# Performance work log

Measured on AMD Instinct MI355X. Metric: run time of the kernel, lower is better.

Reference implementation:

```python
import jax, jax.numpy as jnp
import numpy as np
from jax import lax

# Faithful JAX port of the approxmatch CUDA kernel (Fan et al. EMD):
#   iterates annealing levels j = 7 .. -2 with level = -4^j (0 at j=-2),
#   alternately normalizing transport weights by remaining source capacity
#   (remainL) and capping by remaining target capacity (remainR).
# Cost = sum over matched pairs of Euclidean (sqrt) distance * match weight.

def _approx_match(xyz1, xyz2):
    # xyz1: (b,n,3), xyz2: (b,m,3)
    b, n, _ = xyz1.shape
    m = xyz2.shape[1]
    # squared pairwise distances (b,n,m) -- computed once, reused every level
    d2 = jnp.sum((xyz1[:, :, None, :] - xyz2[:, None, :, :]) ** 2, axis=-1)
    # CUDA kernel capacities: multiL = max(1, m/n), multiR = max(1, n/m) (int ratios)
    multiL = float(max(1, m // n))
    multiR = float(max(1, n // m))
    remainL = jnp.full((b, n), multiL, dtype=xyz1.dtype)
    remainR = jnp.full((b, m), multiR, dtype=xyz1.dtype)
    match = jnp.zeros((b, n, m), dtype=xyz1.dtype)

    # levels for j = 7..-1 are -4^j; j = -2 uses level = 0
    levels = jnp.concatenate([
        -(4.0 ** jnp.arange(7, -2, -1, dtype=jnp.float32)),
        jnp.zeros((1,), jnp.float32),
    ])

    def body(carry, level):
        match, remainL, remainR = carry
        w = jnp.exp(level * d2) * remainR[:, None, :]                 # (b,n,m)
        w = w * (remainL / (1e-9 + w.sum(axis=2)))[:, :, None]        # normalize rows, scale by L capacity
        r = jnp.minimum(remainR / (1e-9 + w.sum(axis=1)), 1.0)        # cap columns by R capacity
        w = w * r[:, None, :]
        match = match + w
        remainL = jnp.maximum(remainL - w.sum(axis=2), 0.0)
        remainR = jnp.maximum(remainR - w.sum(axis=1), 0.0)
        return (match, remainL, remainR), None

    (match, _, _), _ = lax.scan(body, (match, remainL, remainR), levels)
    return match, d2


def _match_cost(match, d2):
    # matchcost kernel: sum_{k,l} match[k,l] * sqrt(||xyz1_k - xyz2_l||^2)
    dist = jnp.sqrt(jnp.maximum(d2, 1e-30))
    return jnp.sum(match * dist, axis=(1, 2))  # (b,)


def setup_inputs() -> dict:
    key = jax.random.key(0)
    k1, k2 = jax.random.split(key)
    b, n, m = 8, 2048, 2048
    input1 = jax.random.uniform(k1, (b, n, 3), dtype=jnp.float32)
    input2 = jax.random.uniform(k2, (b, m, 3), dtype=jnp.float32)
    return {"input1": input1, "input2": input2}


def reference(input1, input2):
    match, d2 = _approx_match(input1, input2)
    return _match_cost(match, d2)  # (b,) per-batch EMD cost
```

## Files before the change

kernel.cpp:

```cpp
#include <hip/hip_runtime.h>
#include <math.h>


#define NPTS 2048
#define BLOCK 256
#define RPW 4
#define RPB ((BLOCK / 64) * RPW)
#define L2E 1.4426950408889634f

__device__ __forceinline__ float xreduce(float v) {
#pragma unroll
    for (int off = 1; off < 64; off <<= 1) v += __shfl_xor(v, off, 64);
    return v;
}
__device__ __forceinline__ float fexp2(float x) { return __builtin_amdgcn_exp2f(x); }
__device__ __forceinline__ float fsqrt(float x) { return __builtin_amdgcn_sqrtf(x); }

__global__ __launch_bounds__(BLOCK, 4) void k_A(
    const float* __restrict__ xyz1, const float* __restrict__ xyz2,
    float4* __restrict__ p1w, float4* __restrict__ p2w,
    float* __restrict__ f_g, float kk, float multiL, float multiR)
{
    __shared__ float sx[NPTS], sy[NPTS], sz[NPTS], sb[NPTS];
    const int row0 = blockIdx.x * RPB;
    const int batch = row0 >> 11;
    const int rloc = row0 & 2047;
    const float* g1 = xyz1 + (size_t)batch * NPTS * 3;
    const float* g2 = xyz2 + (size_t)batch * NPTS * 3;
    if (threadIdx.x < RPB) {
        int i = rloc + threadIdx.x;
        p1w[((size_t)batch << 11) + i] = make_float4(g1[3*i], g1[3*i+1], g1[3*i+2], 0.f);
    } else if (threadIdx.x < 2 * RPB) {
        int i = rloc + threadIdx.x - RPB;
        p2w[((size_t)batch << 11) + i] = make_float4(g2[3*i], g2[3*i+1], g2[3*i+2], 0.f);
    }
    for (int j = threadIdx.x; j < NPTS; j += BLOCK) {
        float qx = g2[3*j], qy = g2[3*j+1], qz = g2[3*j+2];
        sx[j] = qx; sy[j] = qy; sz[j] = qz;
        sb[j] = kk * (qx*qx + qy*qy + qz*qz);
    }
    __syncthreads();
    const int lane = threadIdx.x & 63;
    const int r0 = row0 + (threadIdx.x >> 6) * RPW;
    float pxp[RPW], pyp[RPW], pzp[RPW], pa[RPW], acc[RPW];
#pragma unroll
    for (int r = 0; r < RPW; ++r) {
        const float* p = g1 + 3 * ((r0 & 2047) + r);
        float x = p[0], y = p[1], z = p[2];
        pa[r] = kk * (x*x + y*y + z*z);
        pxp[r] = -2.f*kk*x; pyp[r] = -2.f*kk*y; pzp[r] = -2.f*kk*z;
        acc[r] = 0.f;
    }
    for (int j = lane; j < NPTS; j += 64) {
        float qx = sx[j], qy = sy[j], qz = sz[j], qb = sb[j];
#pragma unroll
        for (int r = 0; r < RPW; ++r) {
            float t = pa[r] + qb;
            t = fmaf(pxp[r], qx, fmaf(pyp[r], qy, fmaf(pzp[r], qz, t)));
            acc[r] += fexp2(t);
        }
    }
#pragma unroll
    for (int r = 0; r < RPW; ++r) {
        float s = multiR * xreduce(acc[r]);
        if (lane == 0) f_g[r0 + r] = multiL / (1e-9f + s);
    }
}

template <bool FIRST>
__global__ __launch_bounds__(BLOCK, 4) void k_B(
    const float4* __restrict__ p1w, const float4* __restrict__ p2w,
    const float* __restrict__ f_g, float* __restrict__ remR,
    float* __restrict__ c_g, float kk, float multiR)
{
    __shared__ float sx[NPTS], sy[NPTS], sz[NPTS], sb[NPTS], sf[NPTS];
    const int col0 = blockIdx.x * RPB;
    const int batch = col0 >> 11;
    const float4* P1 = p1w + ((size_t)batch << 11);
    const float* F = f_g + ((size_t)batch << 11);
    for (int i = threadIdx.x; i < NPTS; i += BLOCK) {
        float4 q = P1[i];
        sx[i] = q.x; sy[i] = q.y; sz[i] = q.z;
        sb[i] = kk * (q.x*q.x + q.y*q.y + q.z*q.z);
        sf[i] = F[i];
    }
    __syncthreads();
    const int lane = threadIdx.x & 63;
    const int c0 = col0 + (threadIdx.x >> 6) * RPW;
    float cxp[RPW], cyp[RPW], czp[RPW], ca[RPW], acc[RPW];
#pragma unroll
    for (int r = 0; r < RPW; ++r) {
        float4 q = p2w[c0 + r];
        ca[r] = kk * (q.x*q.x + q.y*q.y + q.z*q.z);
        cxp[r] = -2.f*kk*q.x; cyp[r] = -2.f*kk*q.y; czp[r] = -2.f*kk*q.z;
        acc[r] = 0.f;
    }
    for (int i = lane; i < NPTS; i += 64) {
        float qx = sx[i], qy = sy[i], qz = sz[i], qb = sb[i], w = sf[i];
#pragma unroll
        for (int r = 0; r < RPW; ++r) {
            float t = ca[r] + qb;
            t = fmaf(cxp[r], qx, fmaf(cyp[r], qy, fmaf(czp[r], qz, t)));
            acc[r] = fmaf(w, fexp2(t), acc[r]);
        }
    }
#pragma unroll
    for (int r = 0; r < RPW; ++r) {
        float s = xreduce(acc[r]);
        if (lane == 0) {
            int gj = c0 + r;
            float R = FIRST ? multiR : remR[gj];
            float colsum = R * s;
            float rr = fminf(R / (1e-9f + colsum), 1.0f);
            c_g[gj] = R * rr;
            remR[gj] = fmaxf(R - colsum * rr, 0.f);
        }
    }
}

template <int MODE, bool FIRSTC>
__global__ __launch_bounds__(BLOCK, 4) void k_CA(
    const float4* __restrict__ p1w, const float4* __restrict__ p2w,
    float* __restrict__ f_g, const float* __restrict__ c_g,
    const float* __restrict__ remR, float* __restrict__ remL,
    float* __restrict__ costrow, float kp, float invkp, float multiL)
{
    __shared__ float sx[NPTS], sy[NPTS], sz[NPTS], sc[NPTS], sr[NPTS];
    const int row0 = blockIdx.x * RPB;
    const int batch = row0 >> 11;
    const float4* P2 = p2w + ((size_t)batch << 11);
    const float* C = c_g + ((size_t)batch << 11);
    const float* R = remR + ((size_t)batch << 11);
    for (int j = threadIdx.x; j < NPTS; j += BLOCK) {
        float4 q = P2[j];
        sx[j] = q.x; sy[j] = q.y; sz[j] = q.z; sc[j] = C[j];
        if (MODE) sr[j] = R[j];
    }
    __syncthreads();
    const int lane = threadIdx.x & 63;
    const int r0 = row0 + (threadIdx.x >> 6) * RPW;
    float pxp[RPW], pyp[RPW], pzp[RPW], pa[RPW];
    float aT[RPW], aU[RPW], aA[RPW];
    float aAs = 0.f;
#pragma unroll
    for (int r = 0; r < RPW; ++r) {
        float4 q = p1w[r0 + r];
        if (MODE == 0) { pxp[r] = q.x; pyp[r] = q.y; pzp[r] = q.z; pa[r] = 0.f; }
        else {
            pa[r] = kp * (q.x*q.x + q.y*q.y + q.z*q.z);
            pxp[r] = -2.f*kp*q.x; pyp[r] = -2.f*kp*q.y; pzp[r] = -2.f*kp*q.z;
        }
        aT[r] = 0.f; aU[r] = 0.f; aA[r] = 0.f;
    }
    for (int j = lane; j < NPTS; j += 64) {
        float qx = sx[j], qy = sy[j], qz = sz[j], cw = sc[j];
        if (MODE == 0) {
#pragma unroll
            for (int r = 0; r < RPW; ++r) {
                float dx = pxp[r] - qx, dy = pyp[r] - qy, dz = pzp[r] - qz;
                float d2 = fmaf(dx, dx, fmaf(dy, dy, dz * dz));
                aT[r] += cw;
                aU[r] = fmaf(cw, fsqrt(d2), aU[r]);
            }
        } else {
            float qb = kp * fmaf(qx, qx, fmaf(qy, qy, qz * qz));
            float rw = sr[j];
            if (MODE == 2) aAs += rw;
#pragma unroll
            for (int r = 0; r < RPW; ++r) {
                float t = pa[r] + qb;
                t = fmaf(pxp[r], qx, fmaf(pyp[r], qy, fmaf(pzp[r], qz, t)));
                float e1 = fexp2(t);
                float e4;
                if (MODE == 1) { float e2 = e1 * e1; e4 = e2 * e2; } else e4 = e1;
                float d2 = fmaxf(t * invkp, 0.f);
                float eC = cw * e4;
                aT[r] += eC;
                aU[r] = fmaf(eC, fsqrt(d2), aU[r]);
                if (MODE == 1) aA[r] = fmaf(rw, e1, aA[r]);
            }
        }
    }
    float aas = (MODE == 2) ? xreduce(aAs) : 0.f;
#pragma unroll
    for (int r = 0; r < RPW; ++r) {
        float tt = xreduce(aT[r]);
        float uu = xreduce(aU[r]);
        float aa = (MODE == 1) ? xreduce(aA[r]) : aas;
        if (lane == 0) {
            int gi = r0 + r;
            float fi = f_g[gi];
            float rl0 = FIRSTC ? multiL : remL[gi];
            float rl = fmaxf(rl0 - fi * tt, 0.f);
            float cst = FIRSTC ? 0.f : costrow[gi];
            costrow[gi] = cst + fi * uu;
            remL[gi] = rl;
            if (MODE) f_g[gi] = rl / (1e-9f + aa);
        }
    }
}

__global__ void k_cost(const float* __restrict__ costrow,
                       float* __restrict__ out, int n) {
    __shared__ float wsum[BLOCK / 64];
    const float* cr = costrow + (size_t)blockIdx.x * n;
    float s = 0.f;
    for (int i = threadIdx.x; i < n; i += BLOCK) s += cr[i];
    s = xreduce(s);
    int wave = threadIdx.x >> 6, lane = threadIdx.x & 63;
    if (lane == 0) wsum[wave] = s;
    __syncthreads();
    if (threadIdx.x == 0) {
        float t = 0.f;
#pragma unroll
        for (int w = 0; w < BLOCK / 64; ++w) t += wsum[w];
        out[blockIdx.x] = t;
    }
}

extern "C" void kernel_launch(void* const* d_in, const int* in_sizes, int n_in,
                              void* d_out, int out_size, void* d_ws, size_t ws_size,
                              hipStream_t stream) {
    const float* xyz1 = (const float*)d_in[0];
    const float* xyz2 = (const float*)d_in[1];
    float* out = (float*)d_out;
    const int b = out_size;
    const int n = in_sizes[0] / (3 * b);
    const int m = in_sizes[1] / (3 * b);
    const int bn = b * n, bm = b * m;

    float4* p1w = (float4*)d_ws;
    float4* p2w = p1w + bn;
    float* remL    = (float*)(p2w + bm);
    float* remR    = remL + bn;
    float* f       = remR + bm;
    float* c       = f + bn;
    float* costrow = c + bm;

    const float multiL = (float)((m / n > 1) ? (m / n) : 1);
    const float multiR = (float)((n / m > 1) ? (n / m) : 1);

    dim3 g(bn / RPB), blk(BLOCK);
    const float kk0 = -16384.f * L2E;
    k_A<<<g, blk, 0, stream>>>(xyz1, xyz2, p1w, p2w, f, kk0, multiL, multiR);

    for (int t = 0; t < 10; ++t) {
        const float lvl = (t < 9) ? -exp2f(2.f * (float)(7 - t)) : 0.f;
        const float kk = lvl * L2E;
        if (t == 0)
            k_B<true><<<g, blk, 0, stream>>>(p1w, p2w, f, remR, c, kk, multiR);
        else
            k_B<false><<<g, blk, 0, stream>>>(p1w, p2w, f, remR, c, kk, multiR);

        if (t == 0) {
            float kp = kk * 0.25f;
            k_CA<1, true><<<g, blk, 0, stream>>>(p1w, p2w, f, c, remR, remL,
                                                 costrow, kp, 1.f / kp, multiL);
        } else if (t < 8) {
            float kp = kk * 0.25f;
            k_CA<1, false><<<g, blk, 0, stream>>>(p1w, p2w, f, c, remR, remL,
                                                  costrow, kp, 1.f / kp, multiL);
        } else if (t == 8) {
            k_CA<2, false><<<g, blk, 0, stream>>>(p1w, p2w, f, c, remR, remL,
                                                  costrow, kk, 1.f / kk, multiL);
        } else {
            k_CA<0, false><<<g, blk, 0, stream>>>(p1w, p2w, f, c, remR, remL,
                                                  costrow, 0.f, 0.f, multiL);
        }
    }
    k_cost<<<dim3(b), blk, 0, stream>>>(costrow, out, n);
}
```

Before: 327.8 us.

## Fuse column-sum pass into row kernel via shared and global atomics

Drops the separate column-pass kernel (k_B) per annealing level. The row kernel now does a second pass that recomputes the exponentials weighted by the new row factors. It reduces these per column in LDS with atomics and accumulates into a double-buffered global sigma array. A thin elementwise kernel then applies the column capping. The level-zero step replaces the per-column work with a broadcast sum, and the final cost reduction is folded into the last row kernel with atomics to the output. In exchange, each row kernel does extra exp work and issues many global atomics, and the summation order is no longer deterministic.

```diff
diff --git a/kernel.cpp b/kernel.cpp
--- a/kernel.cpp
+++ b/kernel.cpp
@@ -5,7 +5,7 @@
 #define NPTS 2048
 #define BLOCK 256
 #define RPW 4
-#define RPB ((BLOCK / 64) * RPW)
+#define RPB 16
 #define L2E 1.4426950408889634f
 
 __device__ __forceinline__ float xreduce(float v) {
@@ -16,12 +16,20 @@
 __device__ __forceinline__ float fexp2(float x) { return __builtin_amdgcn_exp2f(x); }
 __device__ __forceinline__ float fsqrt(float x) { return __builtin_amdgcn_sqrtf(x); }
 
-__global__ __launch_bounds__(BLOCK, 4) void k_A(
+__global__ void k_zero(float* __restrict__ sig2, float* __restrict__ out,
+                       int nsig, int nout) {
+    int i = blockIdx.x * BLOCK + threadIdx.x;
+    if (i < nsig) sig2[i] = 0.f;
+    if (i < nout) out[i] = 0.f;
+}
+
+__global__ __launch_bounds__(BLOCK, 4) void k_A0(
     const float* __restrict__ xyz1, const float* __restrict__ xyz2,
     float4* __restrict__ p1w, float4* __restrict__ p2w,
-    float* __restrict__ f_g, float kk, float multiL, float multiR)
+    float* __restrict__ f_g, float* __restrict__ sig,
+    float kk, float multiL, float multiR)
 {
-    __shared__ float sx[NPTS], sy[NPTS], sz[NPTS], sb[NPTS];
+    __shared__ float sx[NPTS], sy[NPTS], sz[NPTS], sm[NPTS];
     const int row0 = blockIdx.x * RPB;
     const int batch = row0 >> 11;
     const int rloc = row0 & 2047;
@@ -35,87 +43,68 @@
         p2w[((size_t)batch << 11) + i] = make_float4(g2[3*i], g2[3*i+1], g2[3*i+2], 0.f);
     }
     for (int j = threadIdx.x; j < NPTS; j += BLOCK) {
-        float qx = g2[3*j], qy = g2[3*j+1], qz = g2[3*j+2];
-        sx[j] = qx; sy[j] = qy; sz[j] = qz;
-        sb[j] = kk * (qx*qx + qy*qy + qz*qz);
+        sx[j] = g2[3*j]; sy[j] = g2[3*j+1]; sz[j] = g2[3*j+2];
+        sm[j] = 0.f;
     }
     __syncthreads();
     const int lane = threadIdx.x & 63;
-    const int r0 = row0 + (threadIdx.x >> 6) * RPW;
-    float pxp[RPW], pyp[RPW], pzp[RPW], pa[RPW], acc[RPW];
-#pragma unroll
-    for (int r = 0; r < RPW; ++r) {
-        const float* p = g1 + 3 * ((r0 & 2047) + r);
+    const int wave = threadIdx.x >> 6;
+    const int r0 = row0 + wave * RPW;
+    float pa[RPW], pxp[RPW], pyp[RPW], pzp[RPW], acc[RPW];
+#pragma unroll
+    for (int r = 0; r < RPW; ++r) {
+        const float* p = g1 + 3 * (rloc + wave * RPW + r);
         float x = p[0], y = p[1], z = p[2];
         pa[r] = kk * (x*x + y*y + z*z);
         pxp[r] = -2.f*kk*x; pyp[r] = -2.f*kk*y; pzp[r] = -2.f*kk*z;
         acc[r] = 0.f;
     }
     for (int j = lane; j < NPTS; j += 64) {
-        float qx = sx[j], qy = sy[j], qz = sz[j], qb = sb[j];
+        float qx = sx[j], qy = sy[j], qz = sz[j];
+        float qb = kk * fmaf(qx, qx, fmaf(qy, qy, qz * qz));
 #pragma unroll
         for (int r = 0; r < RPW; ++r) {
-            float t = pa[r] + qb;
-            t = fmaf(pxp[r], qx, fmaf(pyp[r], qy, fmaf(pzp[r], qz, t)));
+            float t = fmaf(pxp[r], qx, fmaf(pyp[r], qy, fmaf(pzp[r], qz, pa[r] + qb)));
             acc[r] += fexp2(t);
         }
     }
+    float fp[RPW];
 #pragma unroll
     for (int r = 0; r < RPW; ++r) {
         float s = multiR * xreduce(acc[r]);
-        if (lane == 0) f_g[r0 + r] = multiL / (1e-9f + s);
-    }
+        fp[r] = multiL / (1e-9f + s);
+        if (lane == 0) f_g[r0 + r] = fp[r];
+    }
+    for (int it = 0; it < NPTS / 64; ++it) {
+        int j = (wave * 512 + it * 64 + lane) & 2047;
+        float qx = sx[j], qy = sy[j], qz = sz[j];
+        float qb = kk * fmaf(qx, qx, fmaf(qy, qy, qz * qz));
+        float part = 0.f;
+#pragma unroll
+        for (int r = 0; r < RPW; ++r) {
+            float t = fmaf(pxp[r], qx, fmaf(pyp[r], qy, fmaf(pzp[r], qz, pa[r] + qb)));
+            part = fmaf(fp[r], fexp2(t), part);
+        }
+        atomicAdd(&sm[j], part);
+    }
+    __syncthreads();
+    float* sg = sig + ((size_t)batch << 11);
+    for (int j = threadIdx.x; j < NPTS; j += BLOCK)
+        atomicAdd(&sg[j], sm[j]);
 }
 
 template <bool FIRST>
-__global__ __launch_bounds__(BLOCK, 4) void k_B(
-    const float4* __restrict__ p1w, const float4* __restrict__ p2w,
-    const float* __restrict__ f_g, float* __restrict__ remR,
-    float* __restrict__ c_g, float kk, float multiR)
+__global__ void k_thin(float* __restrict__ sig, float* __restrict__ remR,
+                       float* __restrict__ c_g, float multiR)
 {
-    __shared__ float sx[NPTS], sy[NPTS], sz[NPTS], sb[NPTS], sf[NPTS];
-    const int col0 = blockIdx.x * RPB;
-    const int batch = col0 >> 11;
-    const float4* P1 = p1w + ((size_t)batch << 11);
-    const float* F = f_g + ((size_t)batch << 11);
-    for (int i = threadIdx.x; i < NPTS; i += BLOCK) {
-        float4 q = P1[i];
-        sx[i] = q.x; sy[i] = q.y; sz[i] = q.z;
-        sb[i] = kk * (q.x*q.x + q.y*q.y + q.z*q.z);
-        sf[i] = F[i];
-    }
-    __syncthreads();
-    const int lane = threadIdx.x & 63;
-    const int c0 = col0 + (threadIdx.x >> 6) * RPW;
-    float cxp[RPW], cyp[RPW], czp[RPW], ca[RPW], acc[RPW];
-#pragma unroll
-    for (int r = 0; r < RPW; ++r) {
-        float4 q = p2w[c0 + r];
-        ca[r] = kk * (q.x*q.x + q.y*q.y + q.z*q.z);
-        cxp[r] = -2.f*kk*q.x; cyp[r] = -2.f*kk*q.y; czp[r] = -2.f*kk*q.z;
-        acc[r] = 0.f;
-    }
-    for (int i = lane; i < NPTS; i += 64) {
-        float qx = sx[i], qy = sy[i], qz = sz[i], qb = sb[i], w = sf[i];
-#pragma unroll
-        for (int r = 0; r < RPW; ++r) {
-            float t = ca[r] + qb;
-            t = fmaf(cxp[r], qx, fmaf(cyp[r], qy, fmaf(czp[r], qz, t)));
-            acc[r] = fmaf(w, fexp2(t), acc[r]);
-        }
-    }
-#pragma unroll
-    for (int r = 0; r < RPW; ++r) {
-        float s = xreduce(acc[r]);
-        if (lane == 0) {
-            int gj = c0 + r;
-            float R = FIRST ? multiR : remR[gj];
-            float colsum = R * s;
-            float rr = fminf(R / (1e-9f + colsum), 1.0f);
-            c_g[gj] = R * rr;
-            remR[gj] = fmaxf(R - colsum * rr, 0.f);
-        }
-    }
+    int idx = blockIdx.x * BLOCK + threadIdx.x;
+    float s = sig[idx];
+    sig[idx] = 0.f;
+    float R = FIRST ? multiR : remR[idx];
+    float colsum = R * s;
+    float rr = fminf(R / (1e-9f + colsum), 1.0f);
+    c_g[idx] = R * rr;
+    remR[idx] = fmaxf(R - colsum * rr, 0.f);
 }
 
 template <int MODE, bool FIRSTC>
@@ -123,7 +112,8 @@
     const float4* __restrict__ p1w, const float4* __restrict__ p2w,
     float* __restrict__ f_g, const float* __restrict__ c_g,
     const float* __restrict__ remR, float* __restrict__ remL,
-    float* __restrict__ costrow, float kp, float invkp, float multiL)
+    float* __restrict__ costrow, float* __restrict__ sig,
+    float kp, float rsqkp, float multiL)
 {
     __shared__ float sx[NPTS], sy[NPTS], sz[NPTS], sc[NPTS], sr[NPTS];
     const int row0 = blockIdx.x * RPB;
@@ -133,89 +123,130 @@
     const float* R = remR + ((size_t)batch << 11);
     for (int j = threadIdx.x; j < NPTS; j += BLOCK) {
         float4 q = P2[j];
+        sx[j] = q.x; sy[j] = q.y; sz[j] = q.z; sc[j] = C[j]; sr[j] = R[j];
+    }
+    __syncthreads();
+    const int lane = threadIdx.x & 63;
+    const int wave = threadIdx.x >> 6;
+    const int r0 = row0 + wave * RPW;
+    float pa[RPW], pxp[RPW], pyp[RPW], pzp[RPW], fi[RPW];
+    float aT[RPW], aU[RPW], aA[RPW], aAs = 0.f;
+#pragma unroll
+    for (int r = 0; r < RPW; ++r) {
+        float4 q = p1w[r0 + r];
+        pa[r] = kp * (q.x*q.x + q.y*q.y + q.z*q.z);
+        pxp[r] = -2.f*kp*q.x; pyp[r] = -2.f*kp*q.y; pzp[r] = -2.f*kp*q.z;
+        fi[r] = f_g[r0 + r];
+        aT[r] = 0.f; aU[r] = 0.f; aA[r] = 0.f;
+    }
+    for (int j = lane; j < NPTS; j += 64) {
+        float qx = sx[j], qy = sy[j], qz = sz[j], cw = sc[j], rw = sr[j];
+        float qb = kp * fmaf(qx, qx, fmaf(qy, qy, qz * qz));
+        if (MODE == 2) aAs += rw;
+#pragma unroll
+        for (int r = 0; r < RPW; ++r) {
+            float t = fmaf(pxp[r], qx, fmaf(pyp[r], qy, fmaf(pzp[r], qz, pa[r] + qb)));
+            float e1 = fexp2(t);
+            float eC;
+            if (MODE == 1) { float e2 = e1 * e1; eC = cw * (e2 * e2); }
+            else           { eC = cw * e1; }
+            aT[r] += eC;
+            aU[r] = fmaf(eC, fsqrt(fabsf(t)), aU[r]);
+            if (MODE == 1) aA[r] = fmaf(rw, e1, aA[r]);
+        }
+    }
+    float aas = (MODE == 2) ? xreduce(aAs) : 0.f;
+    float fp[RPW];
+#pragma unroll
+    for (int r = 0; r < RPW; ++r) {
+        float tt = xreduce(aT[r]);
+        float uu = xreduce(aU[r]) * rsqkp;
+        float aa = (MODE == 1) ? xreduce(aA[r]) : aas;
+        int gi = r0 + r;
+        float rl0 = FIRSTC ? multiL : remL[gi];
+        float rl = fmaxf(rl0 - fi[r] * tt, 0.f);
+        fp[r] = rl / (1e-9f + aa);
+        if (lane == 0) {
+            costrow[gi] = (FIRSTC ? 0.f : costrow[gi]) + fi[r] * uu;
+            remL[gi] = rl;
+            f_g[gi] = fp[r];
+        }
+    }
+    __syncthreads();
+    for (int j = threadIdx.x; j < NPTS; j += BLOCK) sc[j] = 0.f;
+    __syncthreads();
+    if (MODE == 1) {
+        for (int it = 0; it < NPTS / 64; ++it) {
+            int j = (wave * 512 + it * 64 + lane) & 2047;
+            float qx = sx[j], qy = sy[j], qz = sz[j];
+            float qb = kp * fmaf(qx, qx, fmaf(qy, qy, qz * qz));
+            float part = 0.f;
+#pragma unroll
+            for (int r = 0; r < RPW; ++r) {
+                float t = fmaf(pxp[r], qx, fmaf(pyp[r], qy, fmaf(pzp[r], qz, pa[r] + qb)));
+                part = fmaf(fp[r], fexp2(t), part);
+            }
+            atomicAdd(&sc[j], part);
+        }
+    } else {
+        if (lane == 0) atomicAdd(&sc[0], fp[0] + fp[1] + fp[2] + fp[3]);
+    }
+    __syncthreads();
+    float* sg = sig + ((size_t)batch << 11);
+    if (MODE == 1) {
+        for (int j = threadIdx.x; j < NPTS; j += BLOCK)
+            atomicAdd(&sg[j], sc[j]);
+    } else {
+        float bc = sc[0];
+        for (int j = threadIdx.x; j < NPTS; j += BLOCK)
+            atomicAdd(&sg[j], bc);
+    }
+}
+
+__global__ __launch_bounds__(BLOCK, 4) void k_C9(
+    const float4* __restrict__ p1w, const float4* __restrict__ p2w,
+    const float* __restrict__ f_g, const float* __restrict__ c_g,
+    const float* __restrict__ costrow, float* __restrict__ out)
+{
+    __shared__ float sx[NPTS], sy[NPTS], sz[NPTS], sc[NPTS];
+    __shared__ float wsum[BLOCK / 64];
+    const int row0 = blockIdx.x * RPB;
+    const int batch = row0 >> 11;
+    const float4* P2 = p2w + ((size_t)batch << 11);
+    const float* C = c_g + ((size_t)batch << 11);
+    for (int j = threadIdx.x; j < NPTS; j += BLOCK) {
+        float4 q = P2[j];
         sx[j] = q.x; sy[j] = q.y; sz[j] = q.z; sc[j] = C[j];
-        if (MODE) sr[j] = R[j];
     }
     __syncthreads();
     const int lane = threadIdx.x & 63;
-    const int r0 = row0 + (threadIdx.x >> 6) * RPW;
-    float pxp[RPW], pyp[RPW], pzp[RPW], pa[RPW];
-    float aT[RPW], aU[RPW], aA[RPW];
-    float aAs = 0.f;
+    const int wave = threadIdx.x >> 6;
+    const int r0 = row0 + wave * RPW;
+    float px[RPW], py[RPW], pz[RPW], aU[RPW];
 #pragma unroll
     for (int r = 0; r < RPW; ++r) {
         float4 q = p1w[r0 + r];
-        if (MODE == 0) { pxp[r] = q.x; pyp[r] = q.y; pzp[r] = q.z; pa[r] = 0.f; }
-        else {
-            pa[r] = kp * (q.x*q.x + q.y*q.y + q.z*q.z);
-            pxp[r] = -2.f*kp*q.x; pyp[r] = -2.f*kp*q.y; pzp[r] = -2.f*kp*q.z;
-        }
-        aT[r] = 0.f; aU[r] = 0.f; aA[r] = 0.f;
+        px[r] = q.x; py[r] = q.y; pz[r] = q.z; aU[r] = 0.f;
     }
     for (int j = lane; j < NPTS; j += 64) {
         float qx = sx[j], qy = sy[j], qz = sz[j], cw = sc[j];
-        if (MODE == 0) {
-#pragma unroll
-            for (int r = 0; r < RPW; ++r) {
-                float dx = pxp[r] - qx, dy = pyp[r] - qy, dz = pzp[r] - qz;
-                float d2 = fmaf(dx, dx, fmaf(dy, dy, dz * dz));
-                aT[r] += cw;
-                aU[r] = fmaf(cw, fsqrt(d2), aU[r]);
-            }
-        } else {
-            float qb = kp * fmaf(qx, qx, fmaf(qy, qy, qz * qz));
-            float rw = sr[j];
-            if (MODE == 2) aAs += rw;
-#pragma unroll
-            for (int r = 0; r < RPW; ++r) {
-                float t = pa[r] + qb;
-                t = fmaf(pxp[r], qx, fmaf(pyp[r], qy, fmaf(pzp[r], qz, t)));
-                float e1 = fexp2(t);
-                float e4;
-                if (MODE == 1) { float e2 = e1 * e1; e4 = e2 * e2; } else e4 = e1;
-                float d2 = fmaxf(t * invkp, 0.f);
-                float eC = cw * e4;
-                aT[r] += eC;
-                aU[r] = fmaf(eC, fsqrt(d2), aU[r]);
-                if (MODE == 1) aA[r] = fmaf(rw, e1, aA[r]);
-            }
-        }
-    }
-    float aas = (MODE == 2) ? xreduce(aAs) : 0.f;
-#pragma unroll
-    for (int r = 0; r < RPW; ++r) {
-        float tt = xreduce(aT[r]);
+#pragma unroll
+        for (int r = 0; r < RPW; ++r) {
+            float dx = px[r] - qx, dy = py[r] - qy, dz = pz[r] - qz;
+            float d2 = fmaf(dx, dx, fmaf(dy, dy, dz * dz));
+            aU[r] = fmaf(cw, fsqrt(d2), aU[r]);
+        }
+    }
+    float psum = 0.f;
+#pragma unroll
+    for (int r = 0; r < RPW; ++r) {
         float uu = xreduce(aU[r]);
-        float aa = (MODE == 1) ? xreduce(aA[r]) : aas;
-        if (lane == 0) {
-            int gi = r0 + r;
-            float fi = f_g[gi];
-            float rl0 = FIRSTC ? multiL : remL[gi];
-            float rl = fmaxf(rl0 - fi * tt, 0.f);
-            float cst = FIRSTC ? 0.f : costrow[gi];
-            costrow[gi] = cst + fi * uu;
-            remL[gi] = rl;
-            if (MODE) f_g[gi] = rl / (1e-9f + aa);
-        }
-    }
-}
-
-__global__ void k_cost(const float* __restrict__ costrow,
-                       float* __restrict__ out, int n) {
-    __shared__ float wsum[BLOCK / 64];
-    const float* cr = costrow + (size_t)blockIdx.x * n;
-    float s = 0.f;
-    for (int i = threadIdx.x; i < n; i += BLOCK) s += cr[i];
-    s = xreduce(s);
-    int wave = threadIdx.x >> 6, lane = threadIdx.x & 63;
-    if (lane == 0) wsum[wave] = s;
-    __syncthreads();
-    if (threadIdx.x == 0) {
-        float t = 0.f;
-#pragma unroll
-        for (int w = 0; w < BLOCK / 64; ++w) t += wsum[w];
-        out[blockIdx.x] = t;
-    }
+        if (lane == 0) psum += costrow[r0 + r] + f_g[r0 + r] * uu;
+    }
+    if (lane == 0) wsum[wave] = psum;
+    __syncthreads();
+    if (threadIdx.x == 0)
+        atomicAdd(&out[batch], wsum[0] + wsum[1] + wsum[2] + wsum[3]);
 }
 
 extern "C" void kernel_launch(void* const* d_in, const int* in_sizes, int n_in,
@@ -231,42 +262,47 @@
 
     float4* p1w = (float4*)d_ws;
     float4* p2w = p1w + bn;
-    float* remL    = (float*)(p2w + bm);
-    float* remR    = remL + bn;
+    float* remR    = (float*)(p2w + bm);
     float* f       = remR + bm;
     float* c       = f + bn;
-    float* costrow = c + bm;
+    float* remL    = c + bm;
+    float* costrow = remL + bn;
+    float* sig     = costrow + bn;
 
     const float multiL = (float)((m / n > 1) ? (m / n) : 1);
     const float multiR = (float)((n / m > 1) ? (n / m) : 1);
 
-    dim3 g(bn / RPB), blk(BLOCK);
+    dim3 blk(BLOCK);
+    dim3 gFat(bn / RPB), gThin(bm / BLOCK);
+
+    k_zero<<<dim3((2 * bm + BLOCK - 1) / BLOCK), blk, 0, stream>>>(sig, out, 2 * bm, b);
+
     const float kk0 = -16384.f * L2E;
-    k_A<<<g, blk, 0, stream>>>(xyz1, xyz2, p1w, p2w, f, kk0, multiL, multiR);
+    k_A0<<<gFat, blk, 0, stream>>>(xyz1, xyz2, p1w, p2w, f, sig, kk0, multiL, multiR);
 
     for (int t = 0; t < 10; ++t) {
-        const float lvl = (t < 9) ? -exp2f(2.f * (float)(7 - t)) : 0.f;
-        const float kk = lvl * L2E;
-        if (t == 0)
-            k_B<true><<<g, blk, 0, stream>>>(p1w, p2w, f, remR, c, kk, multiR);
-        else
-            k_B<false><<<g, blk, 0, stream>>>(p1w, p2w, f, remR, c, kk, multiR);
-
-        if (t == 0) {
-            float kp = kk * 0.25f;
-            k_CA<1, true><<<g, blk, 0, stream>>>(p1w, p2w, f, c, remR, remL,
-                                                 costrow, kp, 1.f / kp, multiL);
-        } else if (t < 8) {
-            float kp = kk * 0.25f;
-            k_CA<1, false><<<g, blk, 0, stream>>>(p1w, p2w, f, c, remR, remL,
-                                                  costrow, kp, 1.f / kp, multiL);
+        float* sigR = sig + (size_t)(t & 1) * bm;
+        float* sigW = sig + (size_t)((t + 1) & 1) * bm;
+        if (t == 0) k_thin<true><<<gThin, blk, 0, stream>>>(sigR, remR, c, multiR);
+        else        k_thin<false><<<gThin, blk, 0, stream>>>(sigR, remR, c, multiR);
+
+        if (t < 8) {
+            const float kk = -exp2f(2.f * (float)(7 - t)) * L2E;
+            const float kp = kk * 0.25f;
+            const float rsq = 1.f / sqrtf(-kp);
+            if (t == 0)
+                k_CA<1, true><<<gFat, blk, 0, stream>>>(p1w, p2w, f, c, remR, remL,
+                                                        costrow, sigW, kp, rsq, multiL);
+            else
+                k_CA<1, false><<<gFat, blk, 0, stream>>>(p1w, p2w, f, c, remR, remL,
+                                                         costrow, sigW, kp, rsq, multiL);
         } else if (t == 8) {
-            k_CA<2, false><<<g, blk, 0, stream>>>(p1w, p2w, f, c, remR, remL,
-                                                  costrow, kk, 1.f / kk, multiL);
+            const float kp = -0.25f * L2E;
+            const float rsq = 1.f / sqrtf(0.25f * L2E);
+            k_CA<2, false><<<gFat, blk, 0, stream>>>(p1w, p2w, f, c, remR, remL,
+                                                     costrow, sigW, kp, rsq, multiL);
         } else {
-            k_CA<0, false><<<g, blk, 0, stream>>>(p1w, p2w, f, c, remR, remL,
-                                                  costrow, 0.f, 0.f, multiL);
-        }
-    }
-    k_cost<<<dim3(b), blk, 0, stream>>>(costrow, out, n);
-}
+            k_C9<<<gFat, blk, 0, stream>>>(p1w, p2w, f, c, costrow, out);
+        }
+    }
+}
```

Measured after the change: 590.3 us. +80.1%, slower.

## Use packed float2 FMAs for exponent terms and fold sqrt scaling out of loop

Applied to the files above, without the earlier changes.

Rewrites the inner loops of the row, column and update kernels to process pairs of rows with two-wide vector FMAs, so the compiler can emit packed FP32 instructions. In the update kernel, the distance is taken as sqrt(|t|) and the 1/sqrt(-kp) factor is applied once after the reduction instead of multiplying by 1/kp per element. It also drops the launch-bounds occupancy hint, adds unroll pragmas, and special-cases the final level kernel. For the t==8 level, the diff recomputes kp on the host as -0.25*L2E and uses the non-squared exponent, so it must still match the original level-1 weights. The absolute-value trick can change rounding near zero distance.

```diff
diff --git a/kernel.cpp b/kernel.cpp
--- a/kernel.cpp
+++ b/kernel.cpp
@@ -4,19 +4,37 @@
 
 #define NPTS 2048
 #define BLOCK 256
-#define RPW 4
-#define RPB ((BLOCK / 64) * RPW)
+#define RPB 16
 #define L2E 1.4426950408889634f
 
+typedef float v2 __attribute__((ext_vector_type(2)));
+
+__device__ __forceinline__ float fexp2(float x) { return __builtin_amdgcn_exp2f(x); }
+__device__ __forceinline__ float fsqrt(float x) { return __builtin_amdgcn_sqrtf(x); }
+__device__ __forceinline__ v2 fma2(v2 a, v2 b, v2 c) { return __builtin_elementwise_fma(a, b, c); }
+__device__ __forceinline__ v2 sp(float a) { v2 r; r.x = a; r.y = a; return r; }
 __device__ __forceinline__ float xreduce(float v) {
 #pragma unroll
     for (int off = 1; off < 64; off <<= 1) v += __shfl_xor(v, off, 64);
     return v;
 }
-__device__ __forceinline__ float fexp2(float x) { return __builtin_amdgcn_exp2f(x); }
-__device__ __forceinline__ float fsqrt(float x) { return __builtin_amdgcn_sqrtf(x); }
-
-__global__ __launch_bounds__(BLOCK, 4) void k_A(
+
+struct RowPair {
+    v2 pa, px, py, pz;
+};
+__device__ __forceinline__ RowPair mk_pair(float4 a, float4 b, float kp) {
+    RowPair r;
+    r.pa = v2{kp * a.w, kp * b.w};
+    r.px = v2{-2.f*kp*a.x, -2.f*kp*b.x};
+    r.py = v2{-2.f*kp*a.y, -2.f*kp*b.y};
+    r.pz = v2{-2.f*kp*a.z, -2.f*kp*b.z};
+    return r;
+}
+__device__ __forceinline__ v2 term(const RowPair& r, float qx, float qy, float qz, v2 qb2) {
+    return fma2(r.px, sp(qx), fma2(r.py, sp(qy), fma2(r.pz, sp(qz), r.pa + qb2)));
+}
+
+__global__ __launch_bounds__(BLOCK) void k_A(
     const float* __restrict__ xyz1, const float* __restrict__ xyz2,
     float4* __restrict__ p1w, float4* __restrict__ p2w,
     float* __restrict__ f_g, float kk, float multiL, float multiR)
@@ -41,34 +59,37 @@
     }
     __syncthreads();
     const int lane = threadIdx.x & 63;
-    const int r0 = row0 + (threadIdx.x >> 6) * RPW;
-    float pxp[RPW], pyp[RPW], pzp[RPW], pa[RPW], acc[RPW];
-#pragma unroll
-    for (int r = 0; r < RPW; ++r) {
-        const float* p = g1 + 3 * ((r0 & 2047) + r);
-        float x = p[0], y = p[1], z = p[2];
-        pa[r] = kk * (x*x + y*y + z*z);
-        pxp[r] = -2.f*kk*x; pyp[r] = -2.f*kk*y; pzp[r] = -2.f*kk*z;
-        acc[r] = 0.f;
-    }
+    const int wave = threadIdx.x >> 6;
+    const int r0 = row0 + wave * 4;
+    RowPair rA, rB;
+    {
+        const float* p = g1 + 3 * ((r0 & 2047));
+        float4 p0 = make_float4(p[0], p[1], p[2], p[0]*p[0]+p[1]*p[1]+p[2]*p[2]);
+        float4 p1 = make_float4(p[3], p[4], p[5], p[3]*p[3]+p[4]*p[4]+p[5]*p[5]);
+        float4 p2 = make_float4(p[6], p[7], p[8], p[6]*p[6]+p[7]*p[7]+p[8]*p[8]);
+        float4 p3 = make_float4(p[9], p[10], p[11], p[9]*p[9]+p[10]*p[10]+p[11]*p[11]);
+        rA = mk_pair(p0, p1, kk); rB = mk_pair(p2, p3, kk);
+    }
+    v2 aSA = sp(0.f), aSB = sp(0.f);
+#pragma unroll 8
     for (int j = lane; j < NPTS; j += 64) {
-        float qx = sx[j], qy = sy[j], qz = sz[j], qb = sb[j];
-#pragma unroll
-        for (int r = 0; r < RPW; ++r) {
-            float t = pa[r] + qb;
-            t = fmaf(pxp[r], qx, fmaf(pyp[r], qy, fmaf(pzp[r], qz, t)));
-            acc[r] += fexp2(t);
-        }
-    }
-#pragma unroll
-    for (int r = 0; r < RPW; ++r) {
-        float s = multiR * xreduce(acc[r]);
-        if (lane == 0) f_g[r0 + r] = multiL / (1e-9f + s);
+        float qx = sx[j], qy = sy[j], qz = sz[j];
+        v2 qb2 = sp(sb[j]);
+        v2 tA = term(rA, qx, qy, qz, qb2);
+        v2 tB = term(rB, qx, qy, qz, qb2);
+        aSA += v2{fexp2(tA.x), fexp2(tA.y)};
+        aSB += v2{fexp2(tB.x), fexp2(tB.y)};
+    }
+    float sv[4] = {xreduce(aSA.x), xreduce(aSA.y), xreduce(aSB.x), xreduce(aSB.y)};
+    if (lane == 0) {
+#pragma unroll
+        for (int r = 0; r < 4; ++r)
+            f_g[r0 + r] = multiL / (1e-9f + multiR * sv[r]);
     }
 }
 
 template <bool FIRST>
-__global__ __launch_bounds__(BLOCK, 4) void k_B(
+__global__ __launch_bounds__(BLOCK) void k_B(
     const float4* __restrict__ p1w, const float4* __restrict__ p2w,
     const float* __restrict__ f_g, float* __restrict__ remR,
     float* __restrict__ c_g, float kk, float multiR)
@@ -86,31 +107,35 @@
     }
     __syncthreads();
     const int lane = threadIdx.x & 63;
-    const int c0 = col0 + (threadIdx.x >> 6) * RPW;
-    float cxp[RPW], cyp[RPW], czp[RPW], ca[RPW], acc[RPW];
-#pragma unroll
-    for (int r = 0; r < RPW; ++r) {
-        float4 q = p2w[c0 + r];
-        ca[r] = kk * (q.x*q.x + q.y*q.y + q.z*q.z);
-        cxp[r] = -2.f*kk*q.x; cyp[r] = -2.f*kk*q.y; czp[r] = -2.f*kk*q.z;
-        acc[r] = 0.f;
-    }
+    const int wave = threadIdx.x >> 6;
+    const int c0 = col0 + wave * 4;
+    RowPair rA, rB;
+    {
+        float4 q0 = p2w[c0], q1 = p2w[c0+1], q2 = p2w[c0+2], q3 = p2w[c0+3];
+        q0.w = q0.x*q0.x + q0.y*q0.y + q0.z*q0.z;
+        q1.w = q1.x*q1.x + q1.y*q1.y + q1.z*q1.z;
+        q2.w = q2.x*q2.x + q2.y*q2.y + q2.z*q2.z;
+        q3.w = q3.x*q3.x + q3.y*q3.y + q3.z*q3.z;
+        rA = mk_pair(q0, q1, kk); rB = mk_pair(q2, q3, kk);
+    }
+    v2 aSA = sp(0.f), aSB = sp(0.f);
+#pragma unroll 8
     for (int i = lane; i < NPTS; i += 64) {
-        float qx = sx[i], qy = sy[i], qz = sz[i], qb = sb[i], w = sf[i];
-#pragma unroll
-        for (int r = 0; r < RPW; ++r) {
-            float t = ca[r] + qb;
-            t = fmaf(cxp[r], qx, fmaf(cyp[r], qy, fmaf(czp[r], qz, t)));
-            acc[r] = fmaf(w, fexp2(t), acc[r]);
-        }
-    }
-#pragma unroll
-    for (int r = 0; r < RPW; ++r) {
-        float s = xreduce(acc[r]);
-        if (lane == 0) {
+        float qx = sx[i], qy = sy[i], qz = sz[i];
+        v2 qb2 = sp(sb[i]);
+        v2 w2 = sp(sf[i]);
+        v2 tA = term(rA, qx, qy, qz, qb2);
+        v2 tB = term(rB, qx, qy, qz, qb2);
+        aSA = fma2(w2, v2{fexp2(tA.x), fexp2(tA.y)}, aSA);
+        aSB = fma2(w2, v2{fexp2(tB.x), fexp2(tB.y)}, aSB);
+    }
+    float sv[4] = {xreduce(aSA.x), xreduce(aSA.y), xreduce(aSB.x), xreduce(aSB.y)};
+    if (lane == 0) {
+#pragma unroll
+        for (int r = 0; r < 4; ++r) {
             int gj = c0 + r;
             float R = FIRST ? multiR : remR[gj];
-            float colsum = R * s;
+            float colsum = R * sv[r];
             float rr = fminf(R / (1e-9f + colsum), 1.0f);
             c_g[gj] = R * rr;
             remR[gj] = fmaxf(R - colsum * rr, 0.f);
@@ -119,11 +144,11 @@
 }
 
 template <int MODE, bool FIRSTC>
-__global__ __launch_bounds__(BLOCK, 4) void k_CA(
+__global__ __launch_bounds__(BLOCK) void k_CA(
     const float4* __restrict__ p1w, const float4* __restrict__ p2w,
     float* __restrict__ f_g, const float* __restrict__ c_g,
     const float* __restrict__ remR, float* __restrict__ remL,
-    float* __restrict__ costrow, float kp, float invkp, float multiL)
+    float* __restrict__ costrow, float kp, float rsqkp, float multiL)
 {
     __shared__ float sx[NPTS], sy[NPTS], sz[NPTS], sc[NPTS], sr[NPTS];
     const int row0 = blockIdx.x * RPB;
@@ -138,64 +163,98 @@
     }
     __syncthreads();
     const int lane = threadIdx.x & 63;
-    const int r0 = row0 + (threadIdx.x >> 6) * RPW;
-    float pxp[RPW], pyp[RPW], pzp[RPW], pa[RPW];
-    float aT[RPW], aU[RPW], aA[RPW];
-    float aAs = 0.f;
-#pragma unroll
-    for (int r = 0; r < RPW; ++r) {
-        float4 q = p1w[r0 + r];
-        if (MODE == 0) { pxp[r] = q.x; pyp[r] = q.y; pzp[r] = q.z; pa[r] = 0.f; }
-        else {
-            pa[r] = kp * (q.x*q.x + q.y*q.y + q.z*q.z);
-            pxp[r] = -2.f*kp*q.x; pyp[r] = -2.f*kp*q.y; pzp[r] = -2.f*kp*q.z;
-        }
-        aT[r] = 0.f; aU[r] = 0.f; aA[r] = 0.f;
-    }
-    for (int j = lane; j < NPTS; j += 64) {
-        float qx = sx[j], qy = sy[j], qz = sz[j], cw = sc[j];
-        if (MODE == 0) {
-#pragma unroll
-            for (int r = 0; r < RPW; ++r) {
-                float dx = pxp[r] - qx, dy = pyp[r] - qy, dz = pzp[r] - qz;
+    const int wave = threadIdx.x >> 6;
+    const int r0 = row0 + wave * 4;
+
+    if (MODE == 0) {
+        float px[4], py[4], pz[4], aU[4];
+#pragma unroll
+        for (int r = 0; r < 4; ++r) {
+            float4 q = p1w[r0 + r];
+            px[r] = q.x; py[r] = q.y; pz[r] = q.z; aU[r] = 0.f;
+        }
+        float aT = 0.f;
+#pragma unroll 4
+        for (int j = lane; j < NPTS; j += 64) {
+            float qx = sx[j], qy = sy[j], qz = sz[j], cw = sc[j];
+            aT += cw;
+#pragma unroll
+            for (int r = 0; r < 4; ++r) {
+                float dx = px[r]-qx, dy = py[r]-qy, dz = pz[r]-qz;
                 float d2 = fmaf(dx, dx, fmaf(dy, dy, dz * dz));
-                aT[r] += cw;
                 aU[r] = fmaf(cw, fsqrt(d2), aU[r]);
             }
+        }
+        float tt = xreduce(aT);
+#pragma unroll
+        for (int r = 0; r < 4; ++r) {
+            float uu = xreduce(aU[r]);
+            if (lane == 0) {
+                int gi = r0 + r;
+                float fi = f_g[gi];
+                remL[gi] = fmaxf(remL[gi] - fi * tt, 0.f);
+                costrow[gi] += fi * uu;
+            }
+        }
+        return;
+    }
+
+    RowPair rA, rB;
+    v2 fiA, fiB;
+    {
+        float4 p0 = p1w[r0], p1 = p1w[r0+1], p2 = p1w[r0+2], p3 = p1w[r0+3];
+        p0.w = p0.x*p0.x + p0.y*p0.y + p0.z*p0.z;
+        p1.w = p1.x*p1.x + p1.y*p1.y + p1.z*p1.z;
+        p2.w = p2.x*p2.x + p2.y*p2.y + p2.z*p2.z;
+        p3.w = p3.x*p3.x + p3.y*p3.y + p3.z*p3.z;
+        rA = mk_pair(p0, p1, kp); rB = mk_pair(p2, p3, kp);
+        fiA = v2{f_g[r0], f_g[r0+1]}; fiB = v2{f_g[r0+2], f_g[r0+3]};
+    }
+    v2 aTA = sp(0.f), aTB = sp(0.f), aUA = sp(0.f), aUB = sp(0.f);
+    v2 aAA = sp(0.f), aAB = sp(0.f);
+    float aAs = 0.f;
+#pragma unroll 4
+    for (int j = lane; j < NPTS; j += 64) {
+        float qx = sx[j], qy = sy[j], qz = sz[j], cw = sc[j], rw = sr[j];
+        v2 qb2 = sp(kp * fmaf(qx, qx, fmaf(qy, qy, qz * qz)));
+        v2 tA = term(rA, qx, qy, qz, qb2);
+        v2 tB = term(rB, qx, qy, qz, qb2);
+        v2 eA = v2{fexp2(tA.x), fexp2(tA.y)};
+        v2 eB = v2{fexp2(tB.x), fexp2(tB.y)};
+        v2 eCA, eCB;
+        if (MODE == 1) {
+            v2 e2A = eA * eA, e2B = eB * eB;
+            eCA = sp(cw) * (e2A * e2A); eCB = sp(cw) * (e2B * e2B);
         } else {
-            float qb = kp * fmaf(qx, qx, fmaf(qy, qy, qz * qz));
-            float rw = sr[j];
-            if (MODE == 2) aAs += rw;
-#pragma unroll
-            for (int r = 0; r < RPW; ++r) {
-                float t = pa[r] + qb;
-                t = fmaf(pxp[r], qx, fmaf(pyp[r], qy, fmaf(pzp[r], qz, t)));
-                float e1 = fexp2(t);
-                float e4;
-                if (MODE == 1) { float e2 = e1 * e1; e4 = e2 * e2; } else e4 = e1;
-                float d2 = fmaxf(t * invkp, 0.f);
-                float eC = cw * e4;
-                aT[r] += eC;
-                aU[r] = fmaf(eC, fsqrt(d2), aU[r]);
-                if (MODE == 1) aA[r] = fmaf(rw, e1, aA[r]);
-            }
-        }
+            eCA = sp(cw) * eA; eCB = sp(cw) * eB;
+        }
+        aTA += eCA; aTB += eCB;
+        v2 stA = v2{fsqrt(fabsf(tA.x)), fsqrt(fabsf(tA.y))};
+        v2 stB = v2{fsqrt(fabsf(tB.x)), fsqrt(fabsf(tB.y))};
+        aUA = fma2(eCA, stA, aUA); aUB = fma2(eCB, stB, aUB);
+        if (MODE == 1) { aAA = fma2(sp(rw), eA, aAA); aAB = fma2(sp(rw), eB, aAB); }
+        else           { aAs += rw; }
     }
     float aas = (MODE == 2) ? xreduce(aAs) : 0.f;
-#pragma unroll
-    for (int r = 0; r < RPW; ++r) {
-        float tt = xreduce(aT[r]);
-        float uu = xreduce(aU[r]);
-        float aa = (MODE == 1) ? xreduce(aA[r]) : aas;
-        if (lane == 0) {
+    float tt[4] = {xreduce(aTA.x), xreduce(aTA.y), xreduce(aTB.x), xreduce(aTB.y)};
+    float uu[4] = {xreduce(aUA.x), xreduce(aUA.y), xreduce(aUB.x), xreduce(aUB.y)};
+    float aav[4];
+    if (MODE == 1) {
+        aav[0] = xreduce(aAA.x); aav[1] = xreduce(aAA.y);
+        aav[2] = xreduce(aAB.x); aav[3] = xreduce(aAB.y);
+    } else {
+        aav[0] = aav[1] = aav[2] = aav[3] = aas;
+    }
+    float fiv[4] = {fiA.x, fiA.y, fiB.x, fiB.y};
+    if (lane == 0) {
+#pragma unroll
+        for (int r = 0; r < 4; ++r) {
             int gi = r0 + r;
-            float fi = f_g[gi];
             float rl0 = FIRSTC ? multiL : remL[gi];
-            float rl = fmaxf(rl0 - fi * tt, 0.f);
-            float cst = FIRSTC ? 0.f : costrow[gi];
-            costrow[gi] = cst + fi * uu;
+            float rl = fmaxf(rl0 - fiv[r] * tt[r], 0.f);
+            costrow[gi] = (FIRSTC ? 0.f : costrow[gi]) + fiv[r] * uu[r] * rsqkp;
             remL[gi] = rl;
-            if (MODE) f_g[gi] = rl / (1e-9f + aa);
+            f_g[gi] = rl / (1e-9f + aav[r]);
         }
     }
 }
@@ -252,20 +311,23 @@
         else
             k_B<false><<<g, blk, 0, stream>>>(p1w, p2w, f, remR, c, kk, multiR);
 
-        if (t == 0) {
-            float kp = kk * 0.25f;
-            k_CA<1, true><<<g, blk, 0, stream>>>(p1w, p2w, f, c, remR, remL,
-                                                 costrow, kp, 1.f / kp, multiL);
-        } else if (t < 8) {
-            float kp = kk * 0.25f;
-            k_CA<1, false><<<g, blk, 0, stream>>>(p1w, p2w, f, c, remR, remL,
-                                                  costrow, kp, 1.f / kp, multiL);
+        if (t < 8) {
+            const float kp = kk * 0.25f;
+            const float rsq = 1.f / sqrtf(-kp);
+            if (t == 0)
+                k_CA<1, true><<<g, blk, 0, stream>>>(p1w, p2w, f, c, remR, remL,
+                                                     costrow, kp, rsq, multiL);
+            else
+                k_CA<1, false><<<g, blk, 0, stream>>>(p1w, p2w, f, c, remR, remL,
+                                                      costrow, kp, rsq, multiL);
         } else if (t == 8) {
+            const float kp = -0.25f * L2E;
+            const float rsq = 1.f / sqrtf(0.25f * L2E);
             k_CA<2, false><<<g, blk, 0, stream>>>(p1w, p2w, f, c, remR, remL,
-                                                  costrow, kk, 1.f / kk, multiL);
+                                                  costrow, kp, rsq, multiL);
         } else {
             k_CA<0, false><<<g, blk, 0, stream>>>(p1w, p2w, f, c, remR, remL,
-                                                  costrow, 0.f, 0.f, multiL);
+                                                  costrow, 0.f, 1.f, multiL);
         }
     }
     k_cost<<<dim3(b), blk, 0, stream>>>(costrow, out, n);
```

Result: faster. 285.7 us (-12.8%).
